# Optimization experiments

Hardware: AMD Instinct MI355X
Metric: run time of the kernel (lower is better)

Reference implementation:

```python
import jax, jax.numpy as jnp
import numpy as np

N_NODES = 100000
N_EDGES = 1600000
D_IN = 128
D_OUT = 128
NUM_NEIGHBORS = 10


def setup_inputs() -> dict:
    key = jax.random.key(0)
    k1, k2, k3, k4 = jax.random.split(key, 4)
    x = jax.random.normal(k1, (N_NODES, D_IN), dtype=jnp.float32)
    edge_index = jax.random.randint(k2, (2, N_EDGES), 0, N_NODES, dtype=jnp.int64)
    W = jax.random.normal(k3, (D_OUT, D_IN), dtype=jnp.float32) / np.sqrt(D_IN)
    b = jax.random.normal(k4, (D_OUT,), dtype=jnp.float32) * 0.01
    return {"x": x, "edge_index": edge_index, "W": W, "b": b}


def reference(x, edge_index, W, b):
    # Torch semantics: for each node, take the FIRST num_neighbors edges
    # (in original edge order) with row==node, mean their col features;
    # fall back to x[node] if the node has no out-edges. Then linear.
    row, col = edge_index[0], edge_index[1]
    N, E = x.shape[0], row.shape[0]
    # Stable sort by row preserves within-row edge order, so "first k per row"
    # is identical to the torch masking loop.
    order = jnp.argsort(row, stable=True)
    row_s = row[order]
    col_s = col[order]
    # Index of first edge of each row segment -> per-edge rank within segment.
    starts = jnp.searchsorted(row_s, jnp.arange(N, dtype=row_s.dtype))
    rank = jnp.arange(E) - starts[row_s]
    keep = (rank < NUM_NEIGHBORS).astype(x.dtype)  # [E]
    # Masked gather + segment sum == sampled neighbor mean numerator.
    feats = x[col_s] * keep[:, None]               # [E, D_IN] (gather-bound)
    sums = jax.ops.segment_sum(feats, row_s, num_segments=N)
    counts = jax.ops.segment_sum(keep, row_s, num_segments=N)  # [N]
    agg = jnp.where(counts[:, None] > 0,
                    sums / jnp.maximum(counts, 1.0)[:, None],
                    x)
    return agg @ W.T + b
```

## Files before the change

### kernel.cpp

```cpp
#include <hip/hip_runtime.h>
#include <hip/hip_bf16.h>
#include <cstdint>
#include <cstddef>

#define D 128
#define KNB 10
#define SENT 0x7FFFFFFF
#define SHIFT 8
#define NPB 256
#define T_BIN 256
#define EPB 4096
#define MAXNB 1024

typedef __attribute__((ext_vector_type(8))) short short8;
typedef __attribute__((ext_vector_type(4))) float floatx4;

__device__ inline unsigned bf16_rne(float f) {
  unsigned u = __builtin_bit_cast(unsigned, f);
  return (u + 0x7FFFu + ((u >> 16) & 1u)) >> 16;
}

__global__ __launch_bounds__(256) void k_init2(int* __restrict__ counts, int NB,
                                               int* __restrict__ slots, int S) {
  int i = blockIdx.x * 256 + threadIdx.x;
  if (i < NB) counts[i] = 0;
  if (i < S) slots[i] = SENT;
}

__global__ __launch_bounds__(T_BIN) void k_count_xcast(const int* __restrict__ row, int E,
                                                       int NB, int* __restrict__ counts,
                                                       int blocks_bin,
                                                       const float* __restrict__ x,
                                                       unsigned* __restrict__ xh, int n8) {
  if ((int)blockIdx.x < blocks_bin) {
    __shared__ int hist[MAXNB];
    for (int i = threadIdx.x; i < NB; i += T_BIN) hist[i] = 0;
    __syncthreads();
    int e0 = blockIdx.x * EPB;
    for (int i = threadIdx.x; i < EPB; i += T_BIN) {
      int e = e0 + i;
      if (e < E) atomicAdd(&hist[row[e] >> SHIFT], 1);
    }
    __syncthreads();
    for (int i = threadIdx.x; i < NB; i += T_BIN)
      if (hist[i]) atomicAdd(&counts[i], hist[i]);
  } else {
    int t = ((int)blockIdx.x - blocks_bin) * T_BIN + threadIdx.x;
    if (t >= n8) return;
    const float4* p = reinterpret_cast<const float4*>(x) + (size_t)t * 2;
    float4 a = p[0], b = p[1];
    uint4 o;
    o.x = bf16_rne(a.x) | (bf16_rne(a.y) << 16);
    o.y = bf16_rne(a.z) | (bf16_rne(a.w) << 16);
    o.z = bf16_rne(b.x) | (bf16_rne(b.y) << 16);
    o.w = bf16_rne(b.z) | (bf16_rne(b.w) << 16);
    reinterpret_cast<uint4*>(xh)[t] = o;
  }
}

__global__ __launch_bounds__(MAXNB) void k_scan(const int* __restrict__ counts, int NB,
                                                int* __restrict__ bases,
                                                int* __restrict__ cursor) {
  __shared__ int buf[MAXNB];
  int t = threadIdx.x;
  int v = (t < NB) ? counts[t] : 0;
  buf[t] = v;
  __syncthreads();
  for (int off = 1; off < MAXNB; off <<= 1) {
    int xv = (t >= off) ? buf[t - off] : 0;
    __syncthreads();
    buf[t] += xv;
    __syncthreads();
  }
  if (t < NB) {
    int base = buf[t] - v;
    bases[t] = base;
    cursor[t] = base;
  }
}

__global__ __launch_bounds__(T_BIN) void k_scatter2(const int* __restrict__ row, int E,
                                                    int NB, int* __restrict__ cursor,
                                                    unsigned* __restrict__ binned) {
  __shared__ int hist[MAXNB];
  __shared__ int lbase[MAXNB];
  for (int i = threadIdx.x; i < NB; i += T_BIN) hist[i] = 0;
  __syncthreads();
  int e0 = blockIdx.x * EPB;
  for (int i = threadIdx.x; i < EPB; i += T_BIN) {
    int e = e0 + i;
    if (e < E) atomicAdd(&hist[row[e] >> SHIFT], 1);
  }
  __syncthreads();
  for (int i = threadIdx.x; i < NB; i += T_BIN) {
    int h = hist[i];
    lbase[i] = h ? atomicAdd(&cursor[i], h) : 0;
  }
  __syncthreads();
  for (int i = threadIdx.x; i < NB; i += T_BIN) hist[i] = 0;
  __syncthreads();
  for (int i = threadIdx.x; i < EPB; i += T_BIN) {
    int e = e0 + i;
    if (e < E) {
      int r = row[e];
      int b = r >> SHIFT;
      int pos = lbase[b] + atomicAdd(&hist[b], 1);
      binned[pos] = ((unsigned)(r & (NPB - 1)) << 24) | (unsigned)e;
    }
  }
}

__global__ __launch_bounds__(256) void k_select(const unsigned* __restrict__ binned,
                                                const int* __restrict__ bases,
                                                const int* __restrict__ counts,
                                                int* __restrict__ slots_g, int N, int E) {
  __shared__ int sl[NPB * KNB];
  int b = blockIdx.x;
  int nbase = b << SHIFT;
  int nloc = min(NPB, N - nbase);
  for (int i = threadIdx.x; i < nloc * KNB; i += 256) sl[i] = SENT;
  __syncthreads();
  int base = bases[b];
  int cnt = counts[b];
  if (cnt > E) cnt = E;
  for (int i = threadIdx.x; i < cnt; i += 256) {
    unsigned en = binned[base + i];
    int rl = (int)(en >> 24);
    int v = (int)(en & 0xFFFFFFu);
    int* s = &sl[rl * KNB];
#pragma unroll
    for (int k = 0; k < KNB; ++k) {
      int old = atomicMin(&s[k], v);
      if (old == SENT) break;
      v = v > old ? v : old;
    }
  }
  __syncthreads();
  for (int i = threadIdx.x; i < nloc * KNB; i += 256)
    slots_g[(size_t)nbase * KNB + i] = sl[i];
}

__global__ __launch_bounds__(256) void k_agg_hb(const unsigned* __restrict__ xh,
                                                const float* __restrict__ x,
                                                const int* __restrict__ ei,
                                                const int* __restrict__ slots,
                                                unsigned* __restrict__ aggbh,
                                                int N, int E) {
  int wave = threadIdx.x >> 6;
  int lane = threadIdx.x & 63;
  int n = blockIdx.x * 4 + wave;
  if (n >= N) return;

  int eid = SENT;
  if (lane < KNB) eid = slots[(size_t)n * KNB + lane];
  bool valid = (lane < KNB) && ((unsigned)eid < (unsigned)E);
  int nsel = __popcll(__ballot(valid));
  int c = valid ? ei[(size_t)E + eid] : -1;

  unsigned uu[KNB];
  float wj[KNB];
#pragma unroll
  for (int j = 0; j < KNB; ++j) {
    int cj = __shfl(c, j);
    bool vj = (unsigned)cj < (unsigned)N;
    wj[j] = vj ? 1.f : 0.f;
    uu[j] = xh[(size_t)(vj ? cj : 0) * 64 + lane];
  }

  float ax = 0.f, ay = 0.f;
  if (nsel > 0) {
#pragma unroll
    for (int j = 0; j < KNB; ++j) {
      ax += wj[j] * __builtin_bit_cast(float, uu[j] << 16);
      ay += wj[j] * __builtin_bit_cast(float, uu[j] & 0xFFFF0000u);
    }
    float sc = 1.f / (float)nsel;
    ax *= sc; ay *= sc;
  } else {
    float2 v = reinterpret_cast<const float2*>(x + (size_t)n * D)[lane];
    ax = v.x; ay = v.y;
  }
  aggbh[(size_t)n * 64 + lane] = bf16_rne(ax) | (bf16_rne(ay) << 16);
}

__global__ __launch_bounds__(256) void k_agg_h(const unsigned* __restrict__ xh,
                                               const float* __restrict__ x,
                                               const int* __restrict__ ei,
                                               const int* __restrict__ slots,
                                               float* __restrict__ agg, int N, int E) {
  int wave = threadIdx.x >> 6;
  int lane = threadIdx.x & 63;
  int n = blockIdx.x * 4 + wave;
  if (n >= N) return;
  int eid = SENT;
  if (lane < KNB) eid = slots[(size_t)n * KNB + lane];
  bool valid = (lane < KNB) && ((unsigned)eid < (unsigned)E);
  unsigned long long m = __ballot(valid);
  int nsel = __popcll(m);
  int c = valid ? ei[(size_t)E + eid] : 0;
  float ax = 0.f, ay = 0.f;
  if (nsel > 0) {
    unsigned long long mm = m;
    while (mm) {
      int j = (int)__builtin_ctzll(mm);
      mm &= mm - 1;
      int cj = __shfl(c, j);
      if ((unsigned)cj >= (unsigned)N) cj = 0;
      unsigned u = xh[(size_t)cj * 64 + lane];
      ax += __builtin_bit_cast(float, u << 16);
      ay += __builtin_bit_cast(float, u & 0xFFFF0000u);
    }
    float sc = 1.f / (float)nsel;
    ax *= sc; ay *= sc;
  } else {
    float2 v = reinterpret_cast<const float2*>(x + (size_t)n * D)[lane];
    ax = v.x; ay = v.y;
  }
  reinterpret_cast<float2*>(agg + (size_t)n * D)[lane] = make_float2(ax, ay);
}

__global__ __launch_bounds__(256) void k_agg(const float* __restrict__ x,
                                             const int* __restrict__ ei,
                                             const int* __restrict__ slots,
                                             float* __restrict__ agg,
                                             int N, int E) {
  int wave = threadIdx.x >> 6;
  int lane = threadIdx.x & 63;
  int n = blockIdx.x * 4 + wave;
  if (n >= N) return;
  int eid = SENT;
  if (lane < KNB) eid = slots[(size_t)n * KNB + lane];
  bool valid = (lane < KNB) && ((unsigned)eid < (unsigned)E);
  unsigned long long m = __ballot(valid);
  int nsel = __popcll(m);
  int c = valid ? ei[(size_t)E + eid] : 0;
  float2 acc = make_float2(0.f, 0.f);
  if (nsel > 0) {
    unsigned long long mm = m;
    while (mm) {
      int j = (int)__builtin_ctzll(mm);
      mm &= mm - 1;
      int cj = __shfl(c, j);
      if ((unsigned)cj >= (unsigned)N) cj = 0;
      float2 v = reinterpret_cast<const float2*>(x + (size_t)cj * D)[lane];
      acc.x += v.x; acc.y += v.y;
    }
    float sc = 1.f / (float)nsel;
    acc.x *= sc; acc.y *= sc;
  } else {
    acc = reinterpret_cast<const float2*>(x + (size_t)n * D)[lane];
  }
  reinterpret_cast<float2*>(agg + (size_t)n * D)[lane] = acc;
}

#define GBN 128
#define LDK 136

__global__ __launch_bounds__(256) void k_gemm_bf(const unsigned short* __restrict__ aggbh,
                                                 const float* __restrict__ Wm,
                                                 const float* __restrict__ bias,
                                                 float* __restrict__ out, int N) {
  __shared__ unsigned short sA[GBN * LDK];
  __shared__ unsigned short sW[GBN * LDK];
  const int tid = threadIdx.x;
  const int n0 = blockIdx.x * GBN;

#pragma unroll
  for (int i = 0; i < 8; ++i) {
    int q = i * 256 + tid;
    int row = q >> 4;
    int c16 = q & 15;
    uint4 v = make_uint4(0u, 0u, 0u, 0u);
    if (n0 + row < N)
      v = reinterpret_cast<const uint4*>(aggbh + (size_t)(n0 + row) * D)[c16];
    *reinterpret_cast<uint4*>(&sA[row * LDK + c16 * 8]) = v;
  }
#pragma unroll
  for (int i = 0; i < 16; ++i) {
    int q = i * 256 + tid;
    int row = q >> 5;
    int c4 = q & 31;
    float4 wv = reinterpret_cast<const float4*>(Wm + (size_t)row * D)[c4];
    ushort4 uw;
    uw.x = (unsigned short)bf16_rne(wv.x);
    uw.y = (unsigned short)bf16_rne(wv.y);
    uw.z = (unsigned short)bf16_rne(wv.z);
    uw.w = (unsigned short)bf16_rne(wv.w);
    *reinterpret_cast<ushort4*>(&sW[row * LDK + c4 * 4]) = uw;
  }
  __syncthreads();

  const int wave = tid >> 6;
  const int lane = tid & 63;
  const int lrow = lane & 15;
  const int quad = lane >> 4;

  floatx4 acc[2][8];
#pragma unroll
  for (int mt = 0; mt < 2; ++mt)
#pragma unroll
    for (int nt = 0; nt < 8; ++nt)
      acc[mt][nt] = (floatx4){0.f, 0.f, 0.f, 0.f};

  float bv[8];
#pragma unroll
  for (int nt = 0; nt < 8; ++nt) bv[nt] = bias[nt * 16 + lrow];

#pragma unroll
  for (int ks = 0; ks < 4; ++ks) {
    int koff = ks * 32 + quad * 8;
    short8 a0 = *reinterpret_cast<const short8*>(&sA[(wave * 32 + lrow) * LDK + koff]);
    short8 a1 = *reinterpret_cast<const short8*>(&sA[(wave * 32 + 16 + lrow) * LDK + koff]);
#pragma unroll
    for (int nt = 0; nt < 8; ++nt) {
      short8 b = *reinterpret_cast<const short8*>(&sW[(nt * 16 + lrow) * LDK + koff]);
      acc[0][nt] = __builtin_amdgcn_mfma_f32_16x16x32_bf16(a0, b, acc[0][nt], 0, 0, 0);
      acc[1][nt] = __builtin_amdgcn_mfma_f32_16x16x32_bf16(a1, b, acc[1][nt], 0, 0, 0);
    }
  }

#pragma unroll
  for (int mt = 0; mt < 2; ++mt) {
    int rbase = n0 + wave * 32 + mt * 16 + quad * 4;
#pragma unroll
    for (int reg = 0; reg < 4; ++reg) {
      int r = rbase + reg;
      if (r < N) {
        float* op = out + (size_t)r * D + lrow;
#pragma unroll
        for (int nt = 0; nt < 8; ++nt)
          op[nt * 16] = acc[mt][nt][reg] + bv[nt];
      }
    }
  }
}

#define BN 128
#define KC 32
#define LDP 132

__global__ __launch_bounds__(256) void k_gemm(const float* __restrict__ agg,
                                              const float* __restrict__ Wm,
                                              const float* __restrict__ bias,
                                              float* __restrict__ out, int N) {
  __shared__ float sA[KC][LDP];
  __shared__ float sW[KC][LDP];
  const int tid = threadIdx.x;
  const int tx = tid & 15;
  const int ty = tid >> 4;
  const int n0 = blockIdx.x * BN;

  float acc[8][8];
#pragma unroll
  for (int i = 0; i < 8; ++i)
#pragma unroll
    for (int j = 0; j < 8; ++j) acc[i][j] = 0.f;

  const int nl = tid >> 3;
  const int kq = tid & 7;

  for (int kc = 0; kc < D; kc += KC) {
#pragma unroll
    for (int i = 0; i < 4; ++i) {
      int rrow = nl + i * 32;
      int n = n0 + rrow;
      float4 av = make_float4(0.f, 0.f, 0.f, 0.f);
      if (n < N)
        av = reinterpret_cast<const float4*>(agg + (size_t)n * D + kc)[kq];
      int k = kq * 4;
      sA[k+0][rrow] = av.x; sA[k+1][rrow] = av.y;
      sA[k+2][rrow] = av.z; sA[k+3][rrow] = av.w;
      float4 wv = reinterpret_cast<const float4*>(Wm + (size_t)rrow * D + kc)[kq];
      sW[k+0][rrow] = wv.x; sW[k+1][rrow] = wv.y;
      sW[k+2][rrow] = wv.z; sW[k+3][rrow] = wv.w;
    }
    __syncthreads();
#pragma unroll
    for (int k = 0; k < KC; ++k) {
      float4 a0 = *reinterpret_cast<const float4*>(&sA[k][ty * 8]);
      float4 a1 = *reinterpret_cast<const float4*>(&sA[k][ty * 8 + 4]);
      float4 w0 = *reinterpret_cast<const float4*>(&sW[k][tx * 8]);
      float4 w1 = *reinterpret_cast<const float4*>(&sW[k][tx * 8 + 4]);
      float a[8] = {a0.x, a0.y, a0.z, a0.w, a1.x, a1.y, a1.z, a1.w};
      float w[8] = {w0.x, w0.y, w0.z, w0.w, w1.x, w1.y, w1.z, w1.w};
#pragma unroll
      for (int i = 0; i < 8; ++i)
#pragma unroll
        for (int j = 0; j < 8; ++j)
          acc[i][j] += a[i] * w[j];
    }
    __syncthreads();
  }

  float4 b0 = reinterpret_cast<const float4*>(bias)[tx * 2];
  float4 b1 = reinterpret_cast<const float4*>(bias)[tx * 2 + 1];
#pragma unroll
  for (int i = 0; i < 8; ++i) {
    int n = n0 + ty * 8 + i;
    if (n < N) {
      float4 v0 = make_float4(acc[i][0] + b0.x, acc[i][1] + b0.y,
                              acc[i][2] + b0.z, acc[i][3] + b0.w);
      float4 v1 = make_float4(acc[i][4] + b1.x, acc[i][5] + b1.y,
                              acc[i][6] + b1.z, acc[i][7] + b1.w);
      float4* op = reinterpret_cast<float4*>(out + (size_t)n * D + tx * 8);
      op[0] = v0;
      op[1] = v1;
    }
  }
}

extern "C" void kernel_launch(void* const* d_in, const int* in_sizes, int n_in,
                              void* d_out, int out_size, void* d_ws, size_t ws_size,
                              hipStream_t stream) {
  const float* x    = (const float*)d_in[0];
  const int*   ei   = (const int*)d_in[1];
  const float* Wm   = (const float*)d_in[2];
  const float* bias = (const float*)d_in[3];
  float* out = (float*)d_out;

  const int N = in_sizes[0] / D;
  const int E = in_sizes[1] / 2;
  const int NB = (N + NPB - 1) >> SHIFT;

  int* counts = (int*)d_ws;
  int* bases  = counts + NB;
  int* cursor = bases + NB;
  size_t off_slots = ((size_t)(3 * NB) * 4 + 15) & ~(size_t)15;
  int* slots = (int*)((char*)d_ws + off_slots);
  size_t off_xh = (off_slots + (size_t)N * KNB * 4 + 15) & ~(size_t)15;
  unsigned* xh = (unsigned*)((char*)d_ws + off_xh);
  size_t off_ab = off_xh + (size_t)N * D * 2;
  unsigned* aggbh = (unsigned*)((char*)d_ws + off_ab);

  const bool have_xh = ws_size >= off_xh + (size_t)N * D * 2;
  const bool have_ab = ws_size >= off_ab + (size_t)N * D * 2;

  unsigned* binned = (unsigned*)d_out;
  const int blocks_bin = (E + EPB - 1) / EPB;
  const int S = N * KNB;
  const int n8 = N * (D / 8);
  const int xblocks = have_xh ? (n8 + T_BIN - 1) / T_BIN : 0;

  k_init2<<<(S + 255) / 256, 256, 0, stream>>>(counts, NB, slots, S);
  k_count_xcast<<<blocks_bin + xblocks, T_BIN, 0, stream>>>(ei, E, NB, counts,
                                                            blocks_bin, x, xh, n8);
  k_scan<<<1, MAXNB, 0, stream>>>(counts, NB, bases, cursor);
  k_scatter2<<<blocks_bin, T_BIN, 0, stream>>>(ei, E, NB, cursor, binned);
  k_select<<<NB, 256, 0, stream>>>(binned, bases, counts, slots, N, E);

  if (have_ab) {
    k_agg_hb<<<(N + 3) / 4, 256, 0, stream>>>(xh, x, ei, slots, aggbh, N, E);
    k_gemm_bf<<<(N + GBN - 1) / GBN, 256, 0, stream>>>(
        (const unsigned short*)aggbh, Wm, bias, out, N);
  } else if (have_xh) {
    k_agg_h<<<(N + 3) / 4, 256, 0, stream>>>(xh, x, ei, slots, out, N, E);
    k_gemm<<<(N + BN - 1) / BN, 256, 0, stream>>>(out, Wm, bias, out, N);
  } else {
    k_agg<<<(N + 3) / 4, 256, 0, stream>>>(x, ei, slots, out, N, E);
    k_gemm<<<(N + BN - 1) / BN, 256, 0, stream>>>(out, Wm, bias, out, N);
  }
}
```

Before: 240.8 us.

## Apply linear transform before aggregation and fuse GEMM into count kernel

Uses linearity of the mean to compute Y = x·Wᵀ in bf16 first, inside the histogram-count launch, so that GEMM overlaps with binning. The aggregation kernel then gathers rows of Y, averages them, adds the bias and writes the final output directly. This removes the separate x-cast pass, the aggregated intermediate buffer and the trailing GEMM kernel. In exchange, Y is rounded to bf16 before averaging, which changes numerical error, and the fallback rows now use bf16 Y instead of the fp32 product.

```diff
diff --git a/kernel.cpp b/kernel.cpp
--- a/kernel.cpp
+++ b/kernel.cpp
@@ -27,11 +27,16 @@
   if (i < S) slots[i] = SENT;
 }
 
-__global__ __launch_bounds__(T_BIN) void k_count_xcast(const int* __restrict__ row, int E,
-                                                       int NB, int* __restrict__ counts,
-                                                       int blocks_bin,
-                                                       const float* __restrict__ x,
-                                                       unsigned* __restrict__ xh, int n8) {
+#define GBN 128
+#define LDK 136
+
+__global__ __launch_bounds__(256) void k_count_gemmY(const int* __restrict__ row, int E,
+                                                     int NB, int* __restrict__ counts,
+                                                     int blocks_bin,
+                                                     const float* __restrict__ x,
+                                                     const float* __restrict__ Wm,
+                                                     unsigned short* __restrict__ yh,
+                                                     int N) {
   if ((int)blockIdx.x < blocks_bin) {
     __shared__ int hist[MAXNB];
     for (int i = threadIdx.x; i < NB; i += T_BIN) hist[i] = 0;
@@ -44,17 +49,76 @@
     __syncthreads();
     for (int i = threadIdx.x; i < NB; i += T_BIN)
       if (hist[i]) atomicAdd(&counts[i], hist[i]);
-  } else {
-    int t = ((int)blockIdx.x - blocks_bin) * T_BIN + threadIdx.x;
-    if (t >= n8) return;
-    const float4* p = reinterpret_cast<const float4*>(x) + (size_t)t * 2;
-    float4 a = p[0], b = p[1];
-    uint4 o;
-    o.x = bf16_rne(a.x) | (bf16_rne(a.y) << 16);
-    o.y = bf16_rne(a.z) | (bf16_rne(a.w) << 16);
-    o.z = bf16_rne(b.x) | (bf16_rne(b.y) << 16);
-    o.w = bf16_rne(b.z) | (bf16_rne(b.w) << 16);
-    reinterpret_cast<uint4*>(xh)[t] = o;
+    return;
+  }
+
+  __shared__ unsigned short sX[GBN * LDK];
+  __shared__ unsigned short sW[GBN * LDK];
+  const int tid = threadIdx.x;
+  const int n0 = ((int)blockIdx.x - blocks_bin) * GBN;
+
+#pragma unroll
+  for (int i = 0; i < 16; ++i) {
+    int q = i * 256 + tid;
+    int r = q >> 5;
+    int c4 = q & 31;
+    float4 xv = make_float4(0.f, 0.f, 0.f, 0.f);
+    if (n0 + r < N)
+      xv = reinterpret_cast<const float4*>(x + (size_t)(n0 + r) * D)[c4];
+    ushort4 ux;
+    ux.x = (unsigned short)bf16_rne(xv.x);
+    ux.y = (unsigned short)bf16_rne(xv.y);
+    ux.z = (unsigned short)bf16_rne(xv.z);
+    ux.w = (unsigned short)bf16_rne(xv.w);
+    *reinterpret_cast<ushort4*>(&sX[r * LDK + c4 * 4]) = ux;
+    float4 wv = reinterpret_cast<const float4*>(Wm + (size_t)r * D)[c4];
+    ushort4 uw;
+    uw.x = (unsigned short)bf16_rne(wv.x);
+    uw.y = (unsigned short)bf16_rne(wv.y);
+    uw.z = (unsigned short)bf16_rne(wv.z);
+    uw.w = (unsigned short)bf16_rne(wv.w);
+    *reinterpret_cast<ushort4*>(&sW[r * LDK + c4 * 4]) = uw;
+  }
+  __syncthreads();
+
+  const int wave = tid >> 6;
+  const int lane = tid & 63;
+  const int lrow = lane & 15;
+  const int quad = lane >> 4;
+
+  floatx4 acc[2][8];
+#pragma unroll
+  for (int mt = 0; mt < 2; ++mt)
+#pragma unroll
+    for (int nt = 0; nt < 8; ++nt)
+      acc[mt][nt] = (floatx4){0.f, 0.f, 0.f, 0.f};
+
+#pragma unroll
+  for (int ks = 0; ks < 4; ++ks) {
+    int koff = ks * 32 + quad * 8;
+    short8 a0 = *reinterpret_cast<const short8*>(&sX[(wave * 32 + lrow) * LDK + koff]);
+    short8 a1 = *reinterpret_cast<const short8*>(&sX[(wave * 32 + 16 + lrow) * LDK + koff]);
+#pragma unroll
+    for (int nt = 0; nt < 8; ++nt) {
+      short8 b = *reinterpret_cast<const short8*>(&sW[(nt * 16 + lrow) * LDK + koff]);
+      acc[0][nt] = __builtin_amdgcn_mfma_f32_16x16x32_bf16(a0, b, acc[0][nt], 0, 0, 0);
+      acc[1][nt] = __builtin_amdgcn_mfma_f32_16x16x32_bf16(a1, b, acc[1][nt], 0, 0, 0);
+    }
+  }
+
+#pragma unroll
+  for (int mt = 0; mt < 2; ++mt) {
+    int rbase = n0 + wave * 32 + mt * 16 + quad * 4;
+#pragma unroll
+    for (int reg = 0; reg < 4; ++reg) {
+      int r = rbase + reg;
+      if (r < N) {
+        unsigned short* op = yh + (size_t)r * D + lrow;
+#pragma unroll
+        for (int nt = 0; nt < 8; ++nt)
+          op[nt * 16] = (unsigned short)bf16_rne(acc[mt][nt][reg]);
+      }
+    }
   }
 }
 
@@ -140,12 +204,12 @@
     slots_g[(size_t)nbase * KNB + i] = sl[i];
 }
 
-__global__ __launch_bounds__(256) void k_agg_hb(const unsigned* __restrict__ xh,
-                                                const float* __restrict__ x,
-                                                const int* __restrict__ ei,
-                                                const int* __restrict__ slots,
-                                                unsigned* __restrict__ aggbh,
-                                                int N, int E) {
+__global__ __launch_bounds__(256) void k_aggY(const unsigned* __restrict__ yh,
+                                              const float* __restrict__ bias,
+                                              const int* __restrict__ ei,
+                                              const int* __restrict__ slots,
+                                              float* __restrict__ out,
+                                              int N, int E) {
   int wave = threadIdx.x >> 6;
   int lane = threadIdx.x & 63;
   int n = blockIdx.x * 4 + wave;
@@ -164,59 +228,27 @@
     int cj = __shfl(c, j);
     bool vj = (unsigned)cj < (unsigned)N;
     wj[j] = vj ? 1.f : 0.f;
-    uu[j] = xh[(size_t)(vj ? cj : 0) * 64 + lane];
-  }
-
-  float ax = 0.f, ay = 0.f;
+    uu[j] = yh[(size_t)(vj ? cj : 0) * 64 + lane];
+  }
+
+  float2 bv = reinterpret_cast<const float2*>(bias)[lane];
+  float ax, ay;
   if (nsel > 0) {
+    ax = 0.f; ay = 0.f;
 #pragma unroll
     for (int j = 0; j < KNB; ++j) {
       ax += wj[j] * __builtin_bit_cast(float, uu[j] << 16);
       ay += wj[j] * __builtin_bit_cast(float, uu[j] & 0xFFFF0000u);
     }
     float sc = 1.f / (float)nsel;
-    ax *= sc; ay *= sc;
+    ax = ax * sc + bv.x;
+    ay = ay * sc + bv.y;
   } else {
-    float2 v = reinterpret_cast<const float2*>(x + (size_t)n * D)[lane];
-    ax = v.x; ay = v.y;
-  }
-  aggbh[(size_t)n * 64 + lane] = bf16_rne(ax) | (bf16_rne(ay) << 16);
-}
-
-__global__ __launch_bounds__(256) void k_agg_h(const unsigned* __restrict__ xh,
-                                               const float* __restrict__ x,
-                                               const int* __restrict__ ei,
-                                               const int* __restrict__ slots,
-                                               float* __restrict__ agg, int N, int E) {
-  int wave = threadIdx.x >> 6;
-  int lane = threadIdx.x & 63;
-  int n = blockIdx.x * 4 + wave;
-  if (n >= N) return;
-  int eid = SENT;
-  if (lane < KNB) eid = slots[(size_t)n * KNB + lane];
-  bool valid = (lane < KNB) && ((unsigned)eid < (unsigned)E);
-  unsigned long long m = __ballot(valid);
-  int nsel = __popcll(m);
-  int c = valid ? ei[(size_t)E + eid] : 0;
-  float ax = 0.f, ay = 0.f;
-  if (nsel > 0) {
-    unsigned long long mm = m;
-    while (mm) {
-      int j = (int)__builtin_ctzll(mm);
-      mm &= mm - 1;
-      int cj = __shfl(c, j);
-      if ((unsigned)cj >= (unsigned)N) cj = 0;
-      unsigned u = xh[(size_t)cj * 64 + lane];
-      ax += __builtin_bit_cast(float, u << 16);
-      ay += __builtin_bit_cast(float, u & 0xFFFF0000u);
-    }
-    float sc = 1.f / (float)nsel;
-    ax *= sc; ay *= sc;
-  } else {
-    float2 v = reinterpret_cast<const float2*>(x + (size_t)n * D)[lane];
-    ax = v.x; ay = v.y;
-  }
-  reinterpret_cast<float2*>(agg + (size_t)n * D)[lane] = make_float2(ax, ay);
+    unsigned u = yh[(size_t)n * 64 + lane];
+    ax = __builtin_bit_cast(float, u << 16) + bv.x;
+    ay = __builtin_bit_cast(float, u & 0xFFFF0000u) + bv.y;
+  }
+  reinterpret_cast<float2*>(out + (size_t)n * D)[lane] = make_float2(ax, ay);
 }
 
 __global__ __launch_bounds__(256) void k_agg(const float* __restrict__ x,
@@ -253,88 +285,6 @@
   reinterpret_cast<float2*>(agg + (size_t)n * D)[lane] = acc;
 }
 
-#define GBN 128
-#define LDK 136
-
-__global__ __launch_bounds__(256) void k_gemm_bf(const unsigned short* __restrict__ aggbh,
-                                                 const float* __restrict__ Wm,
-                                                 const float* __restrict__ bias,
-                                                 float* __restrict__ out, int N) {
-  __shared__ unsigned short sA[GBN * LDK];
-  __shared__ unsigned short sW[GBN * LDK];
-  const int tid = threadIdx.x;
-  const int n0 = blockIdx.x * GBN;
-
-#pragma unroll
-  for (int i = 0; i < 8; ++i) {
-    int q = i * 256 + tid;
-    int row = q >> 4;
-    int c16 = q & 15;
-    uint4 v = make_uint4(0u, 0u, 0u, 0u);
-    if (n0 + row < N)
-      v = reinterpret_cast<const uint4*>(aggbh + (size_t)(n0 + row) * D)[c16];
-    *reinterpret_cast<uint4*>(&sA[row * LDK + c16 * 8]) = v;
-  }
-#pragma unroll
-  for (int i = 0; i < 16; ++i) {
-    int q = i * 256 + tid;
-    int row = q >> 5;
-    int c4 = q & 31;
-    float4 wv = reinterpret_cast<const float4*>(Wm + (size_t)row * D)[c4];
-    ushort4 uw;
-    uw.x = (unsigned short)bf16_rne(wv.x);
-    uw.y = (unsigned short)bf16_rne(wv.y);
-    uw.z = (unsigned short)bf16_rne(wv.z);
-    uw.w = (unsigned short)bf16_rne(wv.w);
-    *reinterpret_cast<ushort4*>(&sW[row * LDK + c4 * 4]) = uw;
-  }
-  __syncthreads();
-
-  const int wave = tid >> 6;
-  const int lane = tid & 63;
-  const int lrow = lane & 15;
-  const int quad = lane >> 4;
-
-  floatx4 acc[2][8];
-#pragma unroll
-  for (int mt = 0; mt < 2; ++mt)
-#pragma unroll
-    for (int nt = 0; nt < 8; ++nt)
-      acc[mt][nt] = (floatx4){0.f, 0.f, 0.f, 0.f};
-
-  float bv[8];
-#pragma unroll
-  for (int nt = 0; nt < 8; ++nt) bv[nt] = bias[nt * 16 + lrow];
-
-#pragma unroll
-  for (int ks = 0; ks < 4; ++ks) {
-    int koff = ks * 32 + quad * 8;
-    short8 a0 = *reinterpret_cast<const short8*>(&sA[(wave * 32 + lrow) * LDK + koff]);
-    short8 a1 = *reinterpret_cast<const short8*>(&sA[(wave * 32 + 16 + lrow) * LDK + koff]);
-#pragma unroll
-    for (int nt = 0; nt < 8; ++nt) {
-      short8 b = *reinterpret_cast<const short8*>(&sW[(nt * 16 + lrow) * LDK + koff]);
-      acc[0][nt] = __builtin_amdgcn_mfma_f32_16x16x32_bf16(a0, b, acc[0][nt], 0, 0, 0);
-      acc[1][nt] = __builtin_amdgcn_mfma_f32_16x16x32_bf16(a1, b, acc[1][nt], 0, 0, 0);
-    }
-  }
-
-#pragma unroll
-  for (int mt = 0; mt < 2; ++mt) {
-    int rbase = n0 + wave * 32 + mt * 16 + quad * 4;
-#pragma unroll
-    for (int reg = 0; reg < 4; ++reg) {
-      int r = rbase + reg;
-      if (r < N) {
-        float* op = out + (size_t)r * D + lrow;
-#pragma unroll
-        for (int nt = 0; nt < 8; ++nt)
-          op[nt * 16] = acc[mt][nt][reg] + bv[nt];
-      }
-    }
-  }
-}
-
 #define BN 128
 #define KC 32
 #define LDP 132
@@ -427,34 +377,26 @@
   int* cursor = bases + NB;
   size_t off_slots = ((size_t)(3 * NB) * 4 + 15) & ~(size_t)15;
   int* slots = (int*)((char*)d_ws + off_slots);
-  size_t off_xh = (off_slots + (size_t)N * KNB * 4 + 15) & ~(size_t)15;
-  unsigned* xh = (unsigned*)((char*)d_ws + off_xh);
-  size_t off_ab = off_xh + (size_t)N * D * 2;
-  unsigned* aggbh = (unsigned*)((char*)d_ws + off_ab);
-
-  const bool have_xh = ws_size >= off_xh + (size_t)N * D * 2;
-  const bool have_ab = ws_size >= off_ab + (size_t)N * D * 2;
+  size_t off_yh = (off_slots + (size_t)N * KNB * 4 + 15) & ~(size_t)15;
+  unsigned short* yh = (unsigned short*)((char*)d_ws + off_yh);
+
+  const bool have_yh = ws_size >= off_yh + (size_t)N * D * 2;
 
   unsigned* binned = (unsigned*)d_out;
   const int blocks_bin = (E + EPB - 1) / EPB;
   const int S = N * KNB;
-  const int n8 = N * (D / 8);
-  const int xblocks = have_xh ? (n8 + T_BIN - 1) / T_BIN : 0;
+  const int gblocks = have_yh ? (N + GBN - 1) / GBN : 0;
 
   k_init2<<<(S + 255) / 256, 256, 0, stream>>>(counts, NB, slots, S);
-  k_count_xcast<<<blocks_bin + xblocks, T_BIN, 0, stream>>>(ei, E, NB, counts,
-                                                            blocks_bin, x, xh, n8);
+  k_count_gemmY<<<blocks_bin + gblocks, T_BIN, 0, stream>>>(ei, E, NB, counts,
+                                                            blocks_bin, x, Wm, yh, N);
   k_scan<<<1, MAXNB, 0, stream>>>(counts, NB, bases, cursor);
   k_scatter2<<<blocks_bin, T_BIN, 0, stream>>>(ei, E, NB, cursor, binned);
   k_select<<<NB, 256, 0, stream>>>(binned, bases, counts, slots, N, E);
 
-  if (have_ab) {
-    k_agg_hb<<<(N + 3) / 4, 256, 0, stream>>>(xh, x, ei, slots, aggbh, N, E);
-    k_gemm_bf<<<(N + GBN - 1) / GBN, 256, 0, stream>>>(
-        (const unsigned short*)aggbh, Wm, bias, out, N);
-  } else if (have_xh) {
-    k_agg_h<<<(N + 3) / 4, 256, 0, stream>>>(xh, x, ei, slots, out, N, E);
-    k_gemm<<<(N + BN - 1) / BN, 256, 0, stream>>>(out, Wm, bias, out, N);
+  if (have_yh) {
+    k_aggY<<<(N + 3) / 4, 256, 0, stream>>>((const unsigned*)yh, bias, ei, slots,
+                                            out, N, E);
   } else {
     k_agg<<<(N + 3) / 4, 256, 0, stream>>>(x, ei, slots, out, N, E);
     k_gemm<<<(N + BN - 1) / BN, 256, 0, stream>>>(out, Wm, bias, out, N);
```

Measured after the change: 249.7 us. +3.7%, slower.
